# Kernel tuning notes

Measured on AMD Instinct MI355X. Metric: run time of the kernel, lower is better.

The kernel has to match this reference:

```python
import jax, jax.numpy as jnp
import numpy as np

B, N, C = 256, 2048, 64      # batch(residues), num_queries/keys(extra MSA seqs), channels
H, KD, VD, OD = 8, 8, 8, 64  # heads, per-head key dim, per-head value dim, output dim


def setup_inputs() -> dict:
    key = jax.random.key(0)
    ks = jax.random.split(key, 9)
    q_data = jax.random.normal(ks[0], (B, N, C), dtype=jnp.float32)
    m_data = jax.random.normal(ks[1], (B, N, C), dtype=jnp.float32)
    # per-sequence 0/1 mask, broadcast across the channel dim (same rank as q_data)
    seq_mask = (jax.random.uniform(ks[2], (B, N, 1)) < 0.9).astype(jnp.float32)
    q_mask = jnp.broadcast_to(seq_mask, (B, N, C))
    bias = jnp.zeros((B, 1, N), dtype=jnp.float32)  # ignored by forward (AF2 quirk)
    q_weights = jax.random.normal(ks[3], (C, H, KD), dtype=jnp.float32) * 0.05
    k_weights = jax.random.normal(ks[4], (C, KD), dtype=jnp.float32) * 0.05
    v_weights = jax.random.normal(ks[5], (C, VD), dtype=jnp.float32) * 0.05
    o_weights = jax.random.normal(ks[6], (H, VD, OD), dtype=jnp.float32) * 0.05
    o_bias = jnp.zeros((OD,), dtype=jnp.float32)
    gating_w = jax.random.normal(ks[7], (C, H, VD), dtype=jnp.float32) * 0.05
    gating_b = jnp.ones((H, VD), dtype=jnp.float32)
    return {
        "q_data": q_data, "m_data": m_data, "q_mask": q_mask, "bias": bias,
        "q_weights": q_weights, "k_weights": k_weights, "v_weights": v_weights,
        "o_weights": o_weights, "o_bias": o_bias,
        "gating_w": gating_w, "gating_b": gating_b,
    }


def reference(q_data, m_data, q_mask, bias, q_weights, k_weights, v_weights,
              o_weights, o_bias, gating_w, gating_b):
    # v, k projections: [B,N,C] x [C,d] -> [B,N,d]
    v = jnp.einsum('bka,ac->bkc', m_data, v_weights)
    k = jnp.einsum('bka,ac->bkc', m_data, k_weights)
    # masked mean over the query axis (dim 1); mask has full channel dim -> factor 1
    q_avg = jnp.sum(q_mask * q_data, axis=1) / (jnp.sum(q_mask, axis=1) + 1e-10)
    # pooled query: [B,C] x [C,H,KD] -> [B,H,KD], scaled by 1/sqrt(per-head key dim)
    q = jnp.einsum('ba,ahc->bhc', q_avg, q_weights) * (KD ** (-0.5))
    # attention bias from mask (the `bias` argument is overwritten, as in the original)
    mask_bias = 1e9 * (q_mask[:, None, :, 0] - 1.0)              # [B,1,N]
    logits = jnp.einsum('bhc,bkc->bhk', q, k) + mask_bias        # [B,H,N]
    weights = jax.nn.softmax(logits, axis=-1)
    weighted_avg = jnp.einsum('bhk,bkc->bhc', weights, v)        # [B,H,VD]
    # sigmoid gating per query
    gate = jax.nn.sigmoid(jnp.einsum('bqc,chv->bqhv', q_data, gating_w) + gating_b)
    gated = weighted_avg[:, None] * gate                          # [B,N,H,VD]
    out = jnp.einsum('bqhc,hco->bqo', gated, o_weights) + o_bias  # [B,N,OD]
    return out
```

## Files before the change

### kernel.cpp

```cpp
#include <hip/hip_runtime.h>
#include <hip/hip_bf16.h>
#include <math.h>

#define BN 256
#define NN 2048
#define CC 64

#define WS_SUMQ 0
#define WS_SUMM (BN * 64)
#define WS_V    (WS_SUMM + BN)
#define WS_S    (WS_V + BN * 64)
#define WS_KQ   (WS_S + BN * 8)
#define WS_MASK (WS_KQ + BN * 512)
#define WS_ZERO_FLOATS WS_KQ

typedef __bf16 bf16x8 __attribute__((ext_vector_type(8)));
typedef float f32x4 __attribute__((ext_vector_type(4)));

__global__ __launch_bounds__(256) void k_pool(const float* __restrict__ qd,
                                              const float* __restrict__ qm,
                                              float* __restrict__ ws) {
    const int b = blockIdx.x >> 2, chunk = blockIdx.x & 3;
    const int tid = threadIdx.x;
    const int r = tid >> 4, c4 = tid & 15;
    const float* qb = qd + (size_t)b * NN * CC;
    const float* mb = qm + (size_t)b * NN * CC;
    float* wmask = ws + WS_MASK + b * NN;

    float4 acc = {0.f, 0.f, 0.f, 0.f};
    float msum = 0.f;
#pragma unroll 4
    for (int i = 0; i < 32; ++i) {
        const int n = chunk * 512 + i * 16 + r;
        const float m = mb[(size_t)n * CC];
        const float4 q4 = *(const float4*)(qb + (size_t)n * CC + c4 * 4);
        acc.x += m * q4.x; acc.y += m * q4.y; acc.z += m * q4.z; acc.w += m * q4.w;
        msum += m;
        if (c4 == 0) wmask[n] = m;
    }

    __shared__ float red[16][64];
    __shared__ float wsum[4];
    red[r][c4 * 4 + 0] = acc.x; red[r][c4 * 4 + 1] = acc.y;
    red[r][c4 * 4 + 2] = acc.z; red[r][c4 * 4 + 3] = acc.w;
    for (int off = 32; off > 0; off >>= 1) msum += __shfl_down(msum, off, 64);
    if ((tid & 63) == 0) wsum[tid >> 6] = msum;
    __syncthreads();
    if (tid < 64) {
        float s = 0.f;
#pragma unroll
        for (int rr = 0; rr < 16; ++rr) s += red[rr][tid];
        atomicAdd(ws + WS_SUMQ + b * 64 + tid, s);
    }
    if (tid == 0) {
        atomicAdd(ws + WS_SUMM + b,
                  (wsum[0] + wsum[1] + wsum[2] + wsum[3]) * (1.f / 16.f));
    }
}

__global__ __launch_bounds__(64) void k_qproj(const float* __restrict__ qw,
                                              const float* __restrict__ kw,
                                              float* __restrict__ ws) {
    const int b = blockIdx.x, t = threadIdx.x;
    __shared__ float qa[64], ql[64];
    const float denom = ws[WS_SUMM + b] + 1e-10f;
    qa[t] = ws[WS_SUMQ + b * 64 + t] / denom;
    __syncthreads();
    float s = 0.f;
#pragma unroll
    for (int c = 0; c < 64; ++c) s += qa[c] * qw[c * 64 + t];
    ql[t] = s * 0.35355339059327373f;
    __syncthreads();
#pragma unroll
    for (int h = 0; h < 8; ++h) {
        float s2 = 0.f;
#pragma unroll
        for (int d = 0; d < 8; ++d) s2 += kw[t * 8 + d] * ql[h * 8 + d];
        ws[WS_KQ + b * 512 + t * 8 + h] = s2;
    }
}

__global__ __launch_bounds__(256) void k_attn(const float* __restrict__ md,
                                              const float* __restrict__ vw,
                                              float* __restrict__ ws) {
    const int b = blockIdx.x >> 2, chunk = blockIdx.x & 3;
    const int tid = threadIdx.x;
    __shared__ float wkv[64][16];
    for (int i = tid; i < 512; i += 256) {
        const int c = i >> 3, d = i & 7;
        wkv[c][d] = ws[WS_KQ + b * 512 + i];
        wkv[c][8 + d] = vw[i];
    }
    __syncthreads();

    const int n0 = chunk * 512 + tid, n1 = n0 + 256;
    float la0[8], va0[8], la1[8], va1[8];
#pragma unroll
    for (int h = 0; h < 8; ++h) { la0[h] = va0[h] = la1[h] = va1[h] = 0.f; }
    const float4* r0 = (const float4*)(md + ((size_t)b * NN + n0) * CC);
    const float4* r1 = (const float4*)(md + ((size_t)b * NN + n1) * CC);
#pragma unroll 4
    for (int c4 = 0; c4 < 16; ++c4) {
        const float4 m0 = r0[c4], m1 = r1[c4];
        const float m0a[4] = {m0.x, m0.y, m0.z, m0.w};
        const float m1a[4] = {m1.x, m1.y, m1.z, m1.w};
#pragma unroll
        for (int j = 0; j < 4; ++j) {
            const int c = c4 * 4 + j;
            const float4* wr = (const float4*)wkv[c];
            const float4 wa = wr[0], wb = wr[1], wc = wr[2], wd = wr[3];
            const float x0 = m0a[j], x1 = m1a[j];
            la0[0] += x0 * wa.x; la0[1] += x0 * wa.y; la0[2] += x0 * wa.z; la0[3] += x0 * wa.w;
            la0[4] += x0 * wb.x; la0[5] += x0 * wb.y; la0[6] += x0 * wb.z; la0[7] += x0 * wb.w;
            va0[0] += x0 * wc.x; va0[1] += x0 * wc.y; va0[2] += x0 * wc.z; va0[3] += x0 * wc.w;
            va0[4] += x0 * wd.x; va0[5] += x0 * wd.y; va0[6] += x0 * wd.z; va0[7] += x0 * wd.w;
            la1[0] += x1 * wa.x; la1[1] += x1 * wa.y; la1[2] += x1 * wa.z; la1[3] += x1 * wa.w;
            la1[4] += x1 * wb.x; la1[5] += x1 * wb.y; la1[6] += x1 * wb.z; la1[7] += x1 * wb.w;
            va1[0] += x1 * wc.x; va1[1] += x1 * wc.y; va1[2] += x1 * wc.z; va1[3] += x1 * wc.w;
            va1[4] += x1 * wd.x; va1[5] += x1 * wd.y; va1[6] += x1 * wd.z; va1[7] += x1 * wd.w;
        }
    }
    const float mk0 = ws[WS_MASK + b * NN + n0];
    const float mk1 = ws[WS_MASK + b * NN + n1];

    __shared__ float P[512][9];
    __shared__ float Vv[512][9];
#pragma unroll
    for (int h = 0; h < 8; ++h) {
        P[tid][h] = mk0 * __expf(la0[h]);
        P[tid + 256][h] = mk1 * __expf(la1[h]);
    }
#pragma unroll
    for (int d = 0; d < 8; ++d) {
        Vv[tid][d] = va0[d];
        Vv[tid + 256][d] = va1[d];
    }
    __syncthreads();
    const int w = tid >> 6, lane = tid & 63, h = lane >> 3, d = lane & 7;
    float acc = 0.f, sacc = 0.f;
    for (int n = w * 128; n < w * 128 + 128; ++n) {
        const float p = P[n][h];
        acc += p * Vv[n][d];
        sacc += p;
    }
    atomicAdd(ws + WS_V + b * 64 + h * 8 + d, acc);
    if (d == 0) atomicAdd(ws + WS_S + b * 8 + h, sacc);
}

__global__ __launch_bounds__(256) void k_out(const float* __restrict__ qd,
                                             const float* __restrict__ ow,
                                             const float* __restrict__ obias,
                                             const float* __restrict__ gw,
                                             const float* __restrict__ gb,
                                             const float* __restrict__ ws,
                                             float* __restrict__ out) {
    const int b = blockIdx.x >> 3, chunk = blockIdx.x & 7;
    const int tid = threadIdx.x;
    const int w = tid >> 6, lane = tid & 63, q16 = lane >> 4, c16 = lane & 15;

    bf16x8 gwf[2][4], w2f[2][4];
    float gbv[4], obv[4];
#pragma unroll
    for (int kc = 0; kc < 2; ++kc) {
        const int k0 = kc * 32 + q16 * 8;
        const float inv_s = 1.f / ws[WS_S + b * 8 + (k0 >> 3)];
#pragma unroll
        for (int t = 0; t < 4; ++t) {
            const int n = t * 16 + c16;
            bf16x8 gf, wf;
#pragma unroll
            for (int j = 0; j < 8; ++j) {
                gf[j] = (__bf16)gw[(size_t)(k0 + j) * 64 + n];
                wf[j] = (__bf16)(ws[WS_V + b * 64 + k0 + j] * inv_s *
                                 ow[(size_t)(k0 + j) * 64 + n]);
            }
            gwf[kc][t] = gf;
            w2f[kc][t] = wf;
        }
    }
#pragma unroll
    for (int t = 0; t < 4; ++t) {
        gbv[t] = gb[t * 16 + c16];
        obv[t] = obias[t * 16 + c16];
    }

    __shared__ __align__(16) __bf16 gl[4][16][72];

    const size_t base_row = (size_t)b * NN + chunk * 256 + w * 16;

    float4 cur0, cur1, cur2, cur3, nxt0, nxt1, nxt2, nxt3;
    {
        const float* arow = qd + (base_row + c16) * CC;
        cur0 = *(const float4*)(arow + q16 * 8);
        cur1 = *(const float4*)(arow + q16 * 8 + 4);
        cur2 = *(const float4*)(arow + 32 + q16 * 8);
        cur3 = *(const float4*)(arow + 32 + q16 * 8 + 4);
    }

    for (int s = 0; s < 4; ++s) {
        if (s < 3) {
            const float* arow = qd + (base_row + (s + 1) * 64 + c16) * CC;
            nxt0 = *(const float4*)(arow + q16 * 8);
            nxt1 = *(const float4*)(arow + q16 * 8 + 4);
            nxt2 = *(const float4*)(arow + 32 + q16 * 8);
            nxt3 = *(const float4*)(arow + 32 + q16 * 8 + 4);
        }
        bf16x8 af[2];
        {
            bf16x8 a;
            a[0] = (__bf16)cur0.x; a[1] = (__bf16)cur0.y; a[2] = (__bf16)cur0.z; a[3] = (__bf16)cur0.w;
            a[4] = (__bf16)cur1.x; a[5] = (__bf16)cur1.y; a[6] = (__bf16)cur1.z; a[7] = (__bf16)cur1.w;
            af[0] = a;
            a[0] = (__bf16)cur2.x; a[1] = (__bf16)cur2.y; a[2] = (__bf16)cur2.z; a[3] = (__bf16)cur2.w;
            a[4] = (__bf16)cur3.x; a[5] = (__bf16)cur3.y; a[6] = (__bf16)cur3.z; a[7] = (__bf16)cur3.w;
            af[1] = a;
        }
        f32x4 accg[4] = {{0.f, 0.f, 0.f, 0.f}, {0.f, 0.f, 0.f, 0.f},
                         {0.f, 0.f, 0.f, 0.f}, {0.f, 0.f, 0.f, 0.f}};
#pragma unroll
        for (int kc = 0; kc < 2; ++kc)
#pragma unroll
            for (int t = 0; t < 4; ++t)
                accg[t] = __builtin_amdgcn_mfma_f32_16x16x32_bf16(af[kc], gwf[kc][t],
                                                                  accg[t], 0, 0, 0);
#pragma unroll
        for (int t = 0; t < 4; ++t)
#pragma unroll
            for (int r2 = 0; r2 < 4; ++r2) {
                const float x = accg[t][r2] + gbv[t];
                const float g = 1.f / (1.f + __expf(-x));
                gl[w][q16 * 4 + r2][t * 16 + c16] = (__bf16)g;
            }
        __asm__ volatile("s_waitcnt lgkmcnt(0)" ::: "memory");
        bf16x8 a2[2];
#pragma unroll
        for (int kc = 0; kc < 2; ++kc)
            a2[kc] = *(const bf16x8*)&gl[w][c16][kc * 32 + q16 * 8];
        f32x4 acco[4] = {{0.f, 0.f, 0.f, 0.f}, {0.f, 0.f, 0.f, 0.f},
                         {0.f, 0.f, 0.f, 0.f}, {0.f, 0.f, 0.f, 0.f}};
#pragma unroll
        for (int kc = 0; kc < 2; ++kc)
#pragma unroll
            for (int t = 0; t < 4; ++t)
                acco[t] = __builtin_amdgcn_mfma_f32_16x16x32_bf16(a2[kc], w2f[kc][t],
                                                                  acco[t], 0, 0, 0);
        __asm__ volatile("s_waitcnt lgkmcnt(0)" ::: "memory");
        float* orow = out + (base_row + s * 64) * CC;
#pragma unroll
        for (int t = 0; t < 4; ++t)
#pragma unroll
            for (int r2 = 0; r2 < 4; ++r2)
                orow[(size_t)(q16 * 4 + r2) * 64 + t * 16 + c16] = acco[t][r2] + obv[t];
        cur0 = nxt0; cur1 = nxt1; cur2 = nxt2; cur3 = nxt3;
    }
}

extern "C" void kernel_launch(void* const* d_in, const int* in_sizes, int n_in,
                              void* d_out, int out_size, void* d_ws, size_t ws_size,
                              hipStream_t stream) {
    const float* q_data = (const float*)d_in[0];
    const float* m_data = (const float*)d_in[1];
    const float* q_mask = (const float*)d_in[2];
    const float* q_w = (const float*)d_in[4];
    const float* k_w = (const float*)d_in[5];
    const float* v_w = (const float*)d_in[6];
    const float* o_w = (const float*)d_in[7];
    const float* o_b = (const float*)d_in[8];
    const float* g_w = (const float*)d_in[9];
    const float* g_b = (const float*)d_in[10];
    float* out = (float*)d_out;
    float* ws = (float*)d_ws;

    hipMemsetAsync(ws, 0, (size_t)WS_ZERO_FLOATS * sizeof(float), stream);
    hipLaunchKernelGGL(k_pool, dim3(BN * 4), dim3(256), 0, stream, q_data, q_mask, ws);
    hipLaunchKernelGGL(k_qproj, dim3(BN), dim3(64), 0, stream, q_w, k_w, ws);
    hipLaunchKernelGGL(k_attn, dim3(BN * 4), dim3(256), 0, stream, m_data, v_w, ws);
    hipLaunchKernelGGL(k_out, dim3(BN * 8), dim3(256), 0, stream, q_data, o_w, o_b,
                       g_w, g_b, ws, out);
}
```

Before: 484.5 us.

## Fuse query projection into attention kernel and replace atomics with per-chunk partials

Removes the memset and the separate k_qproj launch. Each attention block now recomputes the pooled query and the k-projection itself. All atomicAdd reductions are replaced by per-chunk partial sums written to the workspace, which the downstream kernels then reduce. Both k_pool and k_attn now use eight chunks per batch instead of four, and their loads are batched up front to raise memory-level parallelism. In exchange, every attention block redundantly recomputes the q-projection and reads more partials.

```diff
diff --git a/kernel.cpp b/kernel.cpp
--- a/kernel.cpp
+++ b/kernel.cpp
@@ -5,14 +5,13 @@
 #define BN 256
 #define NN 2048
 #define CC 64
+#define NCH 8
 
 #define WS_SUMQ 0
-#define WS_SUMM (BN * 64)
-#define WS_V    (WS_SUMM + BN)
-#define WS_S    (WS_V + BN * 64)
-#define WS_KQ   (WS_S + BN * 8)
-#define WS_MASK (WS_KQ + BN * 512)
-#define WS_ZERO_FLOATS WS_KQ
+#define WS_SUMM (WS_SUMQ + BN * NCH * 64)
+#define WS_V    (WS_SUMM + BN * NCH)
+#define WS_S    (WS_V + BN * NCH * 64)
+#define WS_MASK (WS_S + BN * NCH * 8)
 
 typedef __bf16 bf16x8 __attribute__((ext_vector_type(8)));
 typedef float f32x4 __attribute__((ext_vector_type(4)));
@@ -20,29 +19,38 @@
 __global__ __launch_bounds__(256) void k_pool(const float* __restrict__ qd,
                                               const float* __restrict__ qm,
                                               float* __restrict__ ws) {
-    const int b = blockIdx.x >> 2, chunk = blockIdx.x & 3;
+    const int b = blockIdx.x >> 3, chunk = blockIdx.x & 7;
     const int tid = threadIdx.x;
     const int r = tid >> 4, c4 = tid & 15;
     const float* qb = qd + (size_t)b * NN * CC;
     const float* mb = qm + (size_t)b * NN * CC;
-    float* wmask = ws + WS_MASK + b * NN;
+    float* wmask = ws + WS_MASK + (size_t)b * NN;
+    const int n0 = chunk * 256;
 
     float4 acc = {0.f, 0.f, 0.f, 0.f};
     float msum = 0.f;
-#pragma unroll 4
-    for (int i = 0; i < 32; ++i) {
-        const int n = chunk * 512 + i * 16 + r;
-        const float m = mb[(size_t)n * CC];
-        const float4 q4 = *(const float4*)(qb + (size_t)n * CC + c4 * 4);
-        acc.x += m * q4.x; acc.y += m * q4.y; acc.z += m * q4.z; acc.w += m * q4.w;
-        msum += m;
-        if (c4 == 0) wmask[n] = m;
+#pragma unroll
+    for (int half = 0; half < 2; ++half) {
+        float4 v[8];
+        float m[8];
+#pragma unroll
+        for (int j = 0; j < 8; ++j) {
+            const int n = n0 + half * 128 + j * 16 + r;
+            v[j] = *(const float4*)(qb + (size_t)n * CC + c4 * 4);
+            m[j] = mb[(size_t)n * CC];
+        }
+#pragma unroll
+        for (int j = 0; j < 8; ++j) {
+            acc.x += m[j] * v[j].x; acc.y += m[j] * v[j].y;
+            acc.z += m[j] * v[j].z; acc.w += m[j] * v[j].w;
+            msum += m[j];
+            if (c4 == 0) wmask[n0 + half * 128 + j * 16 + r] = m[j];
+        }
     }
 
     __shared__ float red[16][64];
     __shared__ float wsum[4];
-    red[r][c4 * 4 + 0] = acc.x; red[r][c4 * 4 + 1] = acc.y;
-    red[r][c4 * 4 + 2] = acc.z; red[r][c4 * 4 + 3] = acc.w;
+    *(float4*)&red[r][c4 * 4] = acc;
     for (int off = 32; off > 0; off >>= 1) msum += __shfl_down(msum, off, 64);
     if ((tid & 63) == 0) wsum[tid >> 6] = msum;
     __syncthreads();
@@ -50,101 +58,112 @@
         float s = 0.f;
 #pragma unroll
         for (int rr = 0; rr < 16; ++rr) s += red[rr][tid];
-        atomicAdd(ws + WS_SUMQ + b * 64 + tid, s);
+        ws[WS_SUMQ + (b * 8 + chunk) * 64 + tid] = s;
     }
     if (tid == 0) {
-        atomicAdd(ws + WS_SUMM + b,
-                  (wsum[0] + wsum[1] + wsum[2] + wsum[3]) * (1.f / 16.f));
+        ws[WS_SUMM + b * 8 + chunk] =
+            (wsum[0] + wsum[1] + wsum[2] + wsum[3]) * (1.f / 16.f);
     }
 }
 
-__global__ __launch_bounds__(64) void k_qproj(const float* __restrict__ qw,
+__global__ __launch_bounds__(256) void k_attn(const float* __restrict__ md,
+                                              const float* __restrict__ qw,
                                               const float* __restrict__ kw,
-                                              float* __restrict__ ws) {
-    const int b = blockIdx.x, t = threadIdx.x;
-    __shared__ float qa[64], ql[64];
-    const float denom = ws[WS_SUMM + b] + 1e-10f;
-    qa[t] = ws[WS_SUMQ + b * 64 + t] / denom;
-    __syncthreads();
-    float s = 0.f;
-#pragma unroll
-    for (int c = 0; c < 64; ++c) s += qa[c] * qw[c * 64 + t];
-    ql[t] = s * 0.35355339059327373f;
-    __syncthreads();
-#pragma unroll
-    for (int h = 0; h < 8; ++h) {
-        float s2 = 0.f;
-#pragma unroll
-        for (int d = 0; d < 8; ++d) s2 += kw[t * 8 + d] * ql[h * 8 + d];
-        ws[WS_KQ + b * 512 + t * 8 + h] = s2;
-    }
-}
-
-__global__ __launch_bounds__(256) void k_attn(const float* __restrict__ md,
                                               const float* __restrict__ vw,
                                               float* __restrict__ ws) {
-    const int b = blockIdx.x >> 2, chunk = blockIdx.x & 3;
+    const int b = blockIdx.x >> 3, chunk = blockIdx.x & 7;
     const int tid = threadIdx.x;
+
+    __shared__ float qa[64], ql[64];
     __shared__ float wkv[64][16];
+    __shared__ float P[256][9];
+    __shared__ float Vv[256][9];
+    __shared__ float partV[4][64];
+    __shared__ float partS[4][8];
+
+    const int n = chunk * 256 + tid;
+    const float* rowp = md + ((size_t)b * NN + n) * CC;
+    const float mk = ws[WS_MASK + (size_t)b * NN + n];
+    float4 buf[8];
+#pragma unroll
+    for (int j = 0; j < 8; ++j) buf[j] = ((const float4*)rowp)[j];
+
+    if (tid < 64) {
+        float s = 0.f, den = 0.f;
+#pragma unroll
+        for (int ch = 0; ch < 8; ++ch) {
+            s += ws[WS_SUMQ + (b * 8 + ch) * 64 + tid];
+            den += ws[WS_SUMM + b * 8 + ch];
+        }
+        qa[tid] = s / (den + 1e-10f);
+    }
+    __syncthreads();
+    if (tid < 64) {
+        float s = 0.f;
+#pragma unroll
+        for (int c = 0; c < 64; ++c) s += qa[c] * qw[c * 64 + tid];
+        ql[tid] = s * 0.35355339059327373f;
+    }
+    __syncthreads();
     for (int i = tid; i < 512; i += 256) {
-        const int c = i >> 3, d = i & 7;
-        wkv[c][d] = ws[WS_KQ + b * 512 + i];
-        wkv[c][8 + d] = vw[i];
-    }
-    __syncthreads();
-
-    const int n0 = chunk * 512 + tid, n1 = n0 + 256;
-    float la0[8], va0[8], la1[8], va1[8];
-#pragma unroll
-    for (int h = 0; h < 8; ++h) { la0[h] = va0[h] = la1[h] = va1[h] = 0.f; }
-    const float4* r0 = (const float4*)(md + ((size_t)b * NN + n0) * CC);
-    const float4* r1 = (const float4*)(md + ((size_t)b * NN + n1) * CC);
-#pragma unroll 4
-    for (int c4 = 0; c4 < 16; ++c4) {
-        const float4 m0 = r0[c4], m1 = r1[c4];
-        const float m0a[4] = {m0.x, m0.y, m0.z, m0.w};
-        const float m1a[4] = {m1.x, m1.y, m1.z, m1.w};
-#pragma unroll
-        for (int j = 0; j < 4; ++j) {
-            const int c = c4 * 4 + j;
-            const float4* wr = (const float4*)wkv[c];
-            const float4 wa = wr[0], wb = wr[1], wc = wr[2], wd = wr[3];
-            const float x0 = m0a[j], x1 = m1a[j];
-            la0[0] += x0 * wa.x; la0[1] += x0 * wa.y; la0[2] += x0 * wa.z; la0[3] += x0 * wa.w;
-            la0[4] += x0 * wb.x; la0[5] += x0 * wb.y; la0[6] += x0 * wb.z; la0[7] += x0 * wb.w;
-            va0[0] += x0 * wc.x; va0[1] += x0 * wc.y; va0[2] += x0 * wc.z; va0[3] += x0 * wc.w;
-            va0[4] += x0 * wd.x; va0[5] += x0 * wd.y; va0[6] += x0 * wd.z; va0[7] += x0 * wd.w;
-            la1[0] += x1 * wa.x; la1[1] += x1 * wa.y; la1[2] += x1 * wa.z; la1[3] += x1 * wa.w;
-            la1[4] += x1 * wb.x; la1[5] += x1 * wb.y; la1[6] += x1 * wb.z; la1[7] += x1 * wb.w;
-            va1[0] += x1 * wc.x; va1[1] += x1 * wc.y; va1[2] += x1 * wc.z; va1[3] += x1 * wc.w;
-            va1[4] += x1 * wd.x; va1[5] += x1 * wd.y; va1[6] += x1 * wd.z; va1[7] += x1 * wd.w;
-        }
-    }
-    const float mk0 = ws[WS_MASK + b * NN + n0];
-    const float mk1 = ws[WS_MASK + b * NN + n1];
-
-    __shared__ float P[512][9];
-    __shared__ float Vv[512][9];
-#pragma unroll
-    for (int h = 0; h < 8; ++h) {
-        P[tid][h] = mk0 * __expf(la0[h]);
-        P[tid + 256][h] = mk1 * __expf(la1[h]);
-    }
-#pragma unroll
-    for (int d = 0; d < 8; ++d) {
-        Vv[tid][d] = va0[d];
-        Vv[tid + 256][d] = va1[d];
-    }
-    __syncthreads();
+        const int c = i >> 3, h = i & 7;
+        float s = 0.f;
+#pragma unroll
+        for (int d = 0; d < 8; ++d) s += kw[c * 8 + d] * ql[h * 8 + d];
+        wkv[c][h] = s;
+        wkv[c][8 + h] = vw[i];
+    }
+    __syncthreads();
+
+    float la[8], va[8];
+#pragma unroll
+    for (int h = 0; h < 8; ++h) { la[h] = 0.f; va[h] = 0.f; }
+#pragma unroll
+    for (int half = 0; half < 2; ++half) {
+        if (half == 1) {
+#pragma unroll
+            for (int j = 0; j < 8; ++j) buf[j] = ((const float4*)rowp)[8 + j];
+        }
+#pragma unroll
+        for (int j = 0; j < 8; ++j) {
+            const float xa[4] = {buf[j].x, buf[j].y, buf[j].z, buf[j].w};
+#pragma unroll
+            for (int q = 0; q < 4; ++q) {
+                const int c = half * 32 + j * 4 + q;
+                const float4* wr = (const float4*)wkv[c];
+                const float4 wa = wr[0], wb = wr[1], wc = wr[2], wd = wr[3];
+                const float x = xa[q];
+                la[0] += x * wa.x; la[1] += x * wa.y; la[2] += x * wa.z; la[3] += x * wa.w;
+                la[4] += x * wb.x; la[5] += x * wb.y; la[6] += x * wb.z; la[7] += x * wb.w;
+                va[0] += x * wc.x; va[1] += x * wc.y; va[2] += x * wc.z; va[3] += x * wc.w;
+                va[4] += x * wd.x; va[5] += x * wd.y; va[6] += x * wd.z; va[7] += x * wd.w;
+            }
+        }
+    }
+
+#pragma unroll
+    for (int h = 0; h < 8; ++h) P[tid][h] = mk * __expf(la[h]);
+#pragma unroll
+    for (int d = 0; d < 8; ++d) Vv[tid][d] = va[d];
+    __syncthreads();
+
     const int w = tid >> 6, lane = tid & 63, h = lane >> 3, d = lane & 7;
     float acc = 0.f, sacc = 0.f;
-    for (int n = w * 128; n < w * 128 + 128; ++n) {
-        const float p = P[n][h];
-        acc += p * Vv[n][d];
+    for (int i = 0; i < 64; ++i) {
+        const int rr = w * 64 + i;
+        const float p = P[rr][h];
+        acc += p * Vv[rr][d];
         sacc += p;
     }
-    atomicAdd(ws + WS_V + b * 64 + h * 8 + d, acc);
-    if (d == 0) atomicAdd(ws + WS_S + b * 8 + h, sacc);
+    partV[w][lane] = acc;
+    if (d == 0) partS[w][h] = sacc;
+    __syncthreads();
+    if (tid < 64)
+        ws[WS_V + (b * 8 + chunk) * 64 + tid] =
+            partV[0][tid] + partV[1][tid] + partV[2][tid] + partV[3][tid];
+    if (tid < 8)
+        ws[WS_S + (b * 8 + chunk) * 8 + tid] =
+            partS[0][tid] + partS[1][tid] + partS[2][tid] + partS[3][tid];
 }
 
 __global__ __launch_bounds__(256) void k_out(const float* __restrict__ qd,
@@ -158,21 +177,37 @@
     const int tid = threadIdx.x;
     const int w = tid >> 6, lane = tid & 63, q16 = lane >> 4, c16 = lane & 15;
 
+    __shared__ float s_wavg[64], s_sden[8];
+    if (tid < 64) {
+        float s = 0.f;
+#pragma unroll
+        for (int ch = 0; ch < 8; ++ch) s += ws[WS_V + (b * 8 + ch) * 64 + tid];
+        s_wavg[tid] = s;
+    }
+    if (tid >= 64 && tid < 72) {
+        const int hh = tid - 64;
+        float s = 0.f;
+#pragma unroll
+        for (int ch = 0; ch < 8; ++ch) s += ws[WS_S + (b * 8 + ch) * 8 + hh];
+        s_sden[hh] = s;
+    }
+    __syncthreads();
+
     bf16x8 gwf[2][4], w2f[2][4];
     float gbv[4], obv[4];
 #pragma unroll
     for (int kc = 0; kc < 2; ++kc) {
         const int k0 = kc * 32 + q16 * 8;
-        const float inv_s = 1.f / ws[WS_S + b * 8 + (k0 >> 3)];
+        const float inv_s = 1.f / s_sden[k0 >> 3];
 #pragma unroll
         for (int t = 0; t < 4; ++t) {
-            const int n = t * 16 + c16;
+            const int n2 = t * 16 + c16;
             bf16x8 gf, wf;
 #pragma unroll
             for (int j = 0; j < 8; ++j) {
-                gf[j] = (__bf16)gw[(size_t)(k0 + j) * 64 + n];
-                wf[j] = (__bf16)(ws[WS_V + b * 64 + k0 + j] * inv_s *
-                                 ow[(size_t)(k0 + j) * 64 + n]);
+                gf[j] = (__bf16)gw[(size_t)(k0 + j) * 64 + n2];
+                wf[j] = (__bf16)(s_wavg[k0 + j] * inv_s *
+                                 ow[(size_t)(k0 + j) * 64 + n2]);
             }
             gwf[kc][t] = gf;
             w2f[kc][t] = wf;
@@ -271,10 +306,9 @@
     float* out = (float*)d_out;
     float* ws = (float*)d_ws;
 
-    hipMemsetAsync(ws, 0, (size_t)WS_ZERO_FLOATS * sizeof(float), stream);
-    hipLaunchKernelGGL(k_pool, dim3(BN * 4), dim3(256), 0, stream, q_data, q_mask, ws);
-    hipLaunchKernelGGL(k_qproj, dim3(BN), dim3(64), 0, stream, q_w, k_w, ws);
-    hipLaunchKernelGGL(k_attn, dim3(BN * 4), dim3(256), 0, stream, m_data, v_w, ws);
-    hipLaunchKernelGGL(k_out, dim3(BN * 8), dim3(256), 0, stream, q_data, o_w, o_b,
+    hipLaunchKernelGGL(k_pool, dim3(BN * NCH), dim3(256), 0, stream, q_data, q_mask, ws);
+    hipLaunchKernelGGL(k_attn, dim3(BN * NCH), dim3(256), 0, stream, m_data, q_w, k_w,
+                       v_w, ws);
+    hipLaunchKernelGGL(k_out, dim3(BN * NCH), dim3(256), 0, stream, q_data, o_w, o_b,
                        g_w, g_b, ws, out);
 }
```

Result: faster. 447.9 us (-7.6%).
